# Kernel tuning notes

Measured on AMD Instinct MI355X. Metric: run time of the kernel, lower is better.

Reference implementation:

```python
import jax, jax.numpy as jnp
import numpy as np

NEG_INF = -1e9


def _rotate_half(x):
    h = x.shape[-1] // 2
    return jnp.concatenate([-x[..., h:], x[..., :h]], axis=-1)


def setup_inputs() -> dict:
    key = jax.random.key(0)
    ks = jax.random.split(key, 6)
    V, P, D, H = 4, 2048, 1280, 16
    hd = D // H
    return {
        "hidden_states": jax.random.normal(ks[0], (V, P, D), jnp.float32),
        "rope_cache": jax.random.normal(ks[1], (V, P, 1, 2 * hd), jnp.float32),
        "valid_lens": jax.random.randint(ks[2], (V,), 0, P, jnp.int32),
        "w_qkv": jax.random.normal(ks[3], (D, 3 * D), jnp.float32) * (D ** -0.5),
        "b_qkv": jnp.zeros((3 * D,), jnp.float32),
        "w_proj": jax.random.normal(ks[4], (D, D), jnp.float32) * (D ** -0.5),
        "b_proj": jnp.zeros((D,), jnp.float32),
        "n_heads": 16,
    }


def reference(hidden_states, rope_cache, valid_lens, w_qkv, b_qkv, w_proj, b_proj, n_heads):
    V, P, D = hidden_states.shape
    H = n_heads
    hd = D // H
    # fused QKV: (V, P, 3, H, hd)
    qkv = (hidden_states @ w_qkv + b_qkv).reshape(V, P, 3, H, hd)
    q, k, v = qkv[:, :, 0], qkv[:, :, 1], qkv[:, :, 2]  # each (V, P, H, hd)
    # 2D RoPE via precomputed cos/sin cache (V, P, 1, 2*hd)
    cos = rope_cache[..., :hd]
    sin = rope_cache[..., hd:]
    q = q * cos + _rotate_half(q) * sin
    k = k * cos + _rotate_half(k) * sin
    # attention with per-vision key padding mask (BlockMask equivalent)
    scale = hd ** -0.5
    scores = jnp.einsum("vqhd,vkhd->vhqk", q, k) * scale
    lens = jnp.maximum(valid_lens, 1)
    key_mask = jnp.arange(P)[None, :] < lens[:, None]  # (V, P)
    scores = jnp.where(key_mask[:, None, None, :], scores, NEG_INF)
    attn = jax.nn.softmax(scores, axis=-1)
    out = jnp.einsum("vhqk,vkhd->vqhd", attn, v).reshape(V, P, D)
    return out @ w_proj + b_proj
```

## Files before the change

### kernel.cpp

```cpp
#include <hip/hip_runtime.h>

typedef unsigned short u16;
typedef short bf16x8 __attribute__((ext_vector_type(8)));
typedef short s16x4 __attribute__((ext_vector_type(4)));
typedef float f32x4 __attribute__((ext_vector_type(4)));

#define DEV __device__ __forceinline__

DEV float b2f(u16 u) { union { unsigned i; float f; } x; x.i = ((unsigned)u) << 16; return x.f; }
DEV u16 f2b(float f) {
  union { float f; unsigned i; } x; x.f = f;
  unsigned r = x.i + 0x7fffu + ((x.i >> 16) & 1u);
  return (u16)(r >> 16);
}

DEV float exp2g(float x) { return __builtin_amdgcn_exp2f(x); }

#define GLDS(gp, lp) __builtin_amdgcn_global_load_lds( \
    (const __attribute__((address_space(1))) void*)(gp), \
    (__attribute__((address_space(3))) void*)(lp), 16, 0, 0)

constexpr float QSCALE = 0.11180339887498949f * 1.4426950408889634f;

__global__ __launch_bounds__(256) void prep_k(const float* __restrict__ hidden,
    u16* __restrict__ Ah, const float* __restrict__ wq, u16* __restrict__ Btq)
{
  __shared__ u16 tile[64 * 40];
  int b = blockIdx.x, tid = threadIdx.x;
  if (b < 5120) {
    int i = (b * 256 + tid) * 8;
    f32x4 a = *(const f32x4*)(hidden + i);
    f32x4 c = *(const f32x4*)(hidden + i + 4);
    bf16x8 o;
#pragma unroll
    for (int j = 0; j < 4; ++j) { o[j] = (short)f2b(a[j]); o[4 + j] = (short)f2b(c[j]); }
    *(bf16x8*)(Ah + i) = o;
  } else {
    int tb = b - 5120;
    int bx = tb % 60, by = tb / 60;
    const int Kd = 1280, Nd = 3840;
    int k0 = by * 32, n0 = bx * 64;
#pragma unroll
    for (int t = 0; t < 2; ++t) {
      int c = t * 256 + tid;
      int k_l = c >> 4, n_l = (c & 15) << 2;
      f32x4 vv = *(const f32x4*)(wq + (size_t)(k0 + k_l) * Nd + n0 + n_l);
#pragma unroll
      for (int j = 0; j < 4; ++j) tile[(n_l + j) * 40 + k_l] = f2b(vv[j]);
    }
    __syncthreads();
    int n_l = tid >> 2, kc = (tid & 3) << 3;
    bf16x8 vv = *(const bf16x8*)(tile + n_l * 40 + kc);
    *(bf16x8*)(Btq + (size_t)(n0 + n_l) * Kd + k0 + kc) = vv;
  }
}

template<int MODE>
__global__ __launch_bounds__(256) void gemm_k(const u16* __restrict__ A,
    const u16* __restrict__ Bt, const float* __restrict__ bias,
    u16* __restrict__ Oq, u16* __restrict__ Ok, u16* __restrict__ Ov,
    float* __restrict__ Of, int M, int N, int K)
{
  __shared__ u16 Asm[128 * 32];
  __shared__ u16 Bsm[128 * 32];
  const int tid = threadIdx.x;
  const int w = tid >> 6, lane = tid & 63, quad = lane >> 4, l16 = lane & 15;
  const int wm = w >> 1, wn = w & 1;
  const int m0 = blockIdx.y * 128, n0 = blockIdx.x * 128;
  const int srow0 = w * 32 + (lane >> 2);
  const int pchunk = lane & 3;

  const f32x4 zero4 = {0.f, 0.f, 0.f, 0.f};
  f32x4 acc[4][4];
#pragma unroll
  for (int i = 0; i < 4; ++i)
#pragma unroll
    for (int j = 0; j < 4; ++j) acc[i][j] = zero4;

  for (int k0 = 0; k0 < K; k0 += 32) {
    __syncthreads();
#pragma unroll
    for (int t = 0; t < 2; ++t) {
      int r = srow0 + t * 16;
      int q = pchunk ^ ((r >> 1) & 3);
      GLDS(A + (size_t)(m0 + r) * K + k0 + q * 8, Asm + r * 32 + pchunk * 8);
      GLDS(Bt + (size_t)(n0 + r) * K + k0 + q * 8, Bsm + r * 32 + pchunk * 8);
    }
    __syncthreads();
    bf16x8 af[4], bfr[4];
#pragma unroll
    for (int mi = 0; mi < 4; ++mi) {
      int lr = wm * 64 + mi * 16 + l16;
      af[mi] = *(const bf16x8*)(Asm + lr * 32 + ((quad ^ ((lr >> 1) & 3)) << 3));
    }
#pragma unroll
    for (int ni = 0; ni < 4; ++ni) {
      int nr = wn * 64 + ni * 16 + l16;
      bfr[ni] = *(const bf16x8*)(Bsm + nr * 32 + ((quad ^ ((nr >> 1) & 3)) << 3));
    }
#pragma unroll
    for (int mi = 0; mi < 4; ++mi)
#pragma unroll
      for (int ni = 0; ni < 4; ++ni)
        acc[mi][ni] = __builtin_amdgcn_mfma_f32_16x16x32_bf16(af[mi], bfr[ni], acc[mi][ni], 0, 0, 0);
  }

#pragma unroll
  for (int mi = 0; mi < 4; ++mi) {
#pragma unroll
    for (int ni = 0; ni < 4; ++ni) {
      int n = n0 + wn * 64 + ni * 16 + l16;
      float bb = bias[n];
#pragma unroll
      for (int r = 0; r < 4; ++r) {
        int m = m0 + wm * 64 + mi * 16 + quad * 4 + r;
        float val = acc[mi][ni][r] + bb;
        if (MODE == 0) {
          int t = n / 1280, rr = n - t * 1280;
          int hh = rr / 80, dd = rr - hh * 80;
          int vv = m >> 11, p = m & 2047;
          int vh = vv * 16 + hh;
          if (t == 0)      Oq[(size_t)(vh * 2048 + p) * 80 + dd] = f2b(val);
          else if (t == 1) Ok[(size_t)(vh * 2048 + p) * 80 + dd] = f2b(val);
          else             Ov[((size_t)vh * 80 + dd) * 2048 + p] = f2b(val);
        } else {
          Of[(size_t)m * N + n] = val;
        }
      }
    }
  }
}

__global__ __launch_bounds__(256) void rope_proj_k(u16* __restrict__ Q, u16* __restrict__ K,
    const float* __restrict__ rope, const float* __restrict__ wp, u16* __restrict__ Btp)
{
  __shared__ u16 tile[64 * 40];
  int b = blockIdx.x, tid = threadIdx.x;
  if (b < 40960) {
    constexpr int TOT = 4 * 16 * 2048 * 40;
    int idx = b * 256 + tid;
    int which = idx >= TOT ? 1 : 0;
    int r = which ? idx - TOT : idx;
    int d = r % 40;
    int t1 = r / 40;
    int p = t1 & 2047;
    int vv = t1 >> 15;
    u16* buf = which ? K : Q;
    size_t base = (size_t)t1 * 80;
    int rc = (vv * 2048 + p) * 160;
    float x0 = b2f(buf[base + d]), x1 = b2f(buf[base + d + 40]);
    float c0 = rope[rc + d], c1 = rope[rc + d + 40];
    float s0 = rope[rc + 80 + d], s1 = rope[rc + 80 + d + 40];
    float y0 = x0 * c0 - x1 * s0;
    float y1 = x1 * c1 + x0 * s1;
    if (!which) { y0 *= QSCALE; y1 *= QSCALE; }
    buf[base + d] = f2b(y0);
    buf[base + d + 40] = f2b(y1);
  } else {
    int tb = b - 40960;
    int bx = tb % 20, by = tb / 20;
    const int Kd = 1280, Nd = 1280;
    int k0 = by * 32, n0 = bx * 64;
#pragma unroll
    for (int t = 0; t < 2; ++t) {
      int c = t * 256 + tid;
      int k_l = c >> 4, n_l = (c & 15) << 2;
      f32x4 vv = *(const f32x4*)(wp + (size_t)(k0 + k_l) * Nd + n0 + n_l);
#pragma unroll
      for (int j = 0; j < 4; ++j) tile[(n_l + j) * 40 + k_l] = f2b(vv[j]);
    }
    __syncthreads();
    int n_l = tid >> 2, kc = (tid & 3) << 3;
    bf16x8 vv = *(const bf16x8*)(tile + n_l * 40 + kc);
    *(bf16x8*)(Btp + (size_t)(n0 + n_l) * Kd + k0 + kc) = vv;
  }
}

__global__ __launch_bounds__(256) void attn_k(const u16* __restrict__ Q,
    const u16* __restrict__ K, const u16* __restrict__ V,
    const int* __restrict__ lens, u16* __restrict__ O, const u16* __restrict__ zbuf)
{
  __shared__ u16 Ksm[64 * 96];
  __shared__ u16 Vt[96 * 64];
  __shared__ u16 Psm[4][16 * 72];
  const int v = blockIdx.z, h = blockIdx.y, q0 = blockIdx.x * 64;
  const int tid = threadIdx.x, w = tid >> 6, lane = tid & 63;
  const int quad = lane >> 4, l16 = lane & 15;
  int len = lens[v]; if (len < 1) len = 1;
  const int vh = v * 16 + h;

  if (tid < 128) {
    int row = 80 + (tid >> 3), pc = tid & 7;
    short val = (row == 80) ? (short)0x3F80 : (short)0;
    bf16x8 v8 = {val, val, val, val, val, val, val, val};
    *(bf16x8*)(Vt + row * 64 + pc * 8) = v8;
  }

  const bf16x8 zero8 = {0, 0, 0, 0, 0, 0, 0, 0};
  bf16x8 qf[3];
  {
    const u16* qp = Q + (size_t)(vh * 2048 + q0 + w * 16 + l16) * 80 + quad * 8;
    qf[0] = *(const bf16x8*)(qp);
    qf[1] = *(const bf16x8*)(qp + 32);
    qf[2] = (quad < 2) ? *(const bf16x8*)(qp + 64) : zero8;
  }

  const u16* kp[3]; int kstr[3];
#pragma unroll
  for (int t = 0; t < 3; ++t) {
    int L = w * 192 + t * 64 + lane;
    int key = L / 12, pc = L - key * 12;
    int q = (pc < 8) ? (pc ^ (key & 7)) : (8 + ((pc - 8) ^ (key & 3)));
    bool valid = q < 10;
    kp[t] = valid ? (K + (size_t)(vh * 2048 + key) * 80 + q * 8) : zbuf;
    kstr[t] = valid ? 5120 : 0;
  }
  const u16* vp[3];
#pragma unroll
  for (int t = 0; t < 3; ++t) {
    int seg = w + t * 4;
    int d = seg * 8 + (lane >> 3), pc = lane & 7;
    int q = pc ^ (d & 7);
    vp[t] = V + ((size_t)vh * 80 + d) * 2048 + q * 8;
  }

  const f32x4 zero4 = {0.f, 0.f, 0.f, 0.f};
  f32x4 o[6];
#pragma unroll
  for (int i = 0; i < 6; ++i) o[i] = zero4;
  float m_run[4] = {-3e38f, -3e38f, -3e38f, -3e38f};

  for (int key0 = 0; key0 < len; key0 += 64) {
    __syncthreads();
#pragma unroll
    for (int t = 0; t < 3; ++t) {
      GLDS(kp[t], Ksm + (w * 192 + t * 64) * 8);
      kp[t] += kstr[t];
    }
#pragma unroll
    for (int t = 0; t < 3; ++t) {
      int seg = w + t * 4;
      if (seg < 10) { GLDS(vp[t], Vt + seg * 512); vp[t] += 64; }
    }
    __syncthreads();

    f32x4 s[4];
#pragma unroll
    for (int i = 0; i < 4; ++i) s[i] = zero4;
#pragma unroll
    for (int ks = 0; ks < 3; ++ks) {
      int ph = (ks < 2) ? ((ks * 4 + quad) ^ (l16 & 7)) : (8 + (quad ^ (l16 & 3)));
#pragma unroll
      for (int ni = 0; ni < 4; ++ni) {
        bf16x8 kb = *(const bf16x8*)(Ksm + (ni * 16 + l16) * 96 + ph * 8);
        s[ni] = __builtin_amdgcn_mfma_f32_16x16x32_bf16(qf[ks], kb, s[ni], 0, 0, 0);
      }
    }
#pragma unroll
    for (int ni = 0; ni < 4; ++ni) {
      int key = key0 + ni * 16 + l16;
      if (key >= len) {
#pragma unroll
        for (int r = 0; r < 4; ++r) s[ni][r] = -1e9f;
      }
    }
    float mx[4];
#pragma unroll
    for (int r = 0; r < 4; ++r) mx[r] = fmaxf(fmaxf(s[0][r], s[1][r]), fmaxf(s[2][r], s[3][r]));
#pragma unroll
    for (int off = 1; off < 16; off <<= 1)
#pragma unroll
      for (int r = 0; r < 4; ++r) mx[r] = fmaxf(mx[r], __shfl_xor(mx[r], off, 64));
    float alpha[4];
#pragma unroll
    for (int r = 0; r < 4; ++r) {
      float mn = fmaxf(m_run[r], mx[r]);
      alpha[r] = exp2g(m_run[r] - mn);
      m_run[r] = mn;
    }
#pragma unroll
    for (int ni = 0; ni < 4; ++ni)
#pragma unroll
      for (int r = 0; r < 4; ++r) s[ni][r] = exp2g(s[ni][r] - m_run[r]);
#pragma unroll
    for (int ni = 0; ni < 4; ++ni)
#pragma unroll
      for (int r = 0; r < 4; ++r) {
        union { float f; unsigned u; } x; x.f = s[ni][r];
        Psm[w][(quad * 4 + r) * 72 + ni * 16 + l16] = (u16)(x.u >> 16);
      }
#pragma unroll
    for (int ni = 0; ni < 6; ++ni)
#pragma unroll
      for (int r = 0; r < 4; ++r) o[ni][r] *= alpha[r];
#pragma unroll
    for (int ks = 0; ks < 2; ++ks) {
      bf16x8 pa = *(const bf16x8*)(&Psm[w][l16 * 72 + ks * 32 + quad * 8]);
      int ph = (ks * 4 + quad) ^ (l16 & 7);
#pragma unroll
      for (int ni = 0; ni < 6; ++ni) {
        bf16x8 vb = *(const bf16x8*)(Vt + (ni * 16 + l16) * 64 + ph * 8);
        o[ni] = __builtin_amdgcn_mfma_f32_16x16x32_bf16(pa, vb, o[ni], 0, 0, 0);
      }
    }
  }
  float inv[4];
#pragma unroll
  for (int r = 0; r < 4; ++r) {
    float l = __shfl(o[5][r], (lane & 48), 64);
    inv[r] = 1.0f / l;
  }
#pragma unroll
  for (int ni = 0; ni < 5; ++ni)
#pragma unroll
    for (int r = 0; r < 4; ++r) {
      int qq = q0 + w * 16 + quad * 4 + r;
      O[((size_t)(v * 2048 + qq) * 16 + h) * 80 + ni * 16 + l16] = f2b(o[ni][r] * inv[r]);
    }
}

extern "C" void kernel_launch(void* const* d_in, const int* in_sizes, int n_in,
                              void* d_out, int out_size, void* d_ws, size_t ws_size,
                              hipStream_t stream) {
  const float* hidden = (const float*)d_in[0];
  const float* rope   = (const float*)d_in[1];
  const int*   lens   = (const int*)d_in[2];
  const float* w_qkv  = (const float*)d_in[3];
  const float* b_qkv  = (const float*)d_in[4];
  const float* w_proj = (const float*)d_in[5];
  const float* b_proj = (const float*)d_in[6];
  float* out = (float*)d_out;
  char* ws = (char*)d_ws;
  u16* Ah = (u16*)(ws);
  u16* Bt = (u16*)(ws + 20971520);
  u16* Qb = (u16*)(ws + 30801920);
  u16* Kb = (u16*)(ws + 51773440);
  u16* Vb = (u16*)(ws + 72744960);
  u16* At = Ah;
  u16* Bp = Bt;

  prep_k<<<7520, 256, 0, stream>>>(hidden, Ah, w_qkv, Bt);
  gemm_k<0><<<dim3(30, 64), 256, 0, stream>>>(Ah, Bt, b_qkv, Qb, Kb, Vb, nullptr, 8192, 3840, 1280);
  rope_proj_k<<<41760, 256, 0, stream>>>(Qb, Kb, rope, w_proj, Bp);
  attn_k<<<dim3(32, 16, 4), 256, 0, stream>>>(Qb, Kb, Vb, lens, At, (const u16*)b_qkv);
  gemm_k<1><<<dim3(10, 64), 256, 0, stream>>>(At, Bp, b_proj, nullptr, nullptr, nullptr, out, 8192, 1280, 1280);
}
```

Baseline: 455.0 us.

## Skip K/V projection tiles past valid length and deepen GEMM K-step to 64

The QKV GEMM now exits early for K and V output tiles whose row block lies entirely beyond the sequence's valid length, because those keys are masked out in attention anyway. Separately, the GEMM K-loop stages 64-wide K slices in LDS with a new 8-way XOR swizzle, halving the number of barrier pairs per tile. This costs twice the LDS per block, which may lower occupancy. The skip is correct only if the attention kernel never reads K/V rows past the clamped length.

```diff
diff --git a/kernel.cpp b/kernel.cpp
--- a/kernel.cpp
+++ b/kernel.cpp
@@ -2,7 +2,6 @@
 
 typedef unsigned short u16;
 typedef short bf16x8 __attribute__((ext_vector_type(8)));
-typedef short s16x4 __attribute__((ext_vector_type(4)));
 typedef float f32x4 __attribute__((ext_vector_type(4)));
 
 #define DEV __device__ __forceinline__
@@ -59,16 +58,24 @@
 __global__ __launch_bounds__(256) void gemm_k(const u16* __restrict__ A,
     const u16* __restrict__ Bt, const float* __restrict__ bias,
     u16* __restrict__ Oq, u16* __restrict__ Ok, u16* __restrict__ Ov,
-    float* __restrict__ Of, int M, int N, int K)
+    float* __restrict__ Of, const int* __restrict__ lens, int M, int N, int K)
 {
-  __shared__ u16 Asm[128 * 32];
-  __shared__ u16 Bsm[128 * 32];
+  __shared__ u16 Asm[128 * 64];
+  __shared__ u16 Bsm[128 * 64];
   const int tid = threadIdx.x;
   const int w = tid >> 6, lane = tid & 63, quad = lane >> 4, l16 = lane & 15;
   const int wm = w >> 1, wn = w & 1;
   const int m0 = blockIdx.y * 128, n0 = blockIdx.x * 128;
-  const int srow0 = w * 32 + (lane >> 2);
-  const int pchunk = lane & 3;
+
+  if (MODE == 0) {
+    if (n0 >= 1280) {
+      int vv = m0 >> 11, p0 = m0 & 2047;
+      int len = lens[vv]; if (len < 1) len = 1;
+      if (p0 >= len) return;
+    }
+  }
+
+  const int srow = tid >> 3, spc = tid & 7;
 
   const f32x4 zero4 = {0.f, 0.f, 0.f, 0.f};
   f32x4 acc[4][4];
@@ -77,32 +84,37 @@
 #pragma unroll
     for (int j = 0; j < 4; ++j) acc[i][j] = zero4;
 
-  for (int k0 = 0; k0 < K; k0 += 32) {
-    __syncthreads();
-#pragma unroll
-    for (int t = 0; t < 2; ++t) {
-      int r = srow0 + t * 16;
-      int q = pchunk ^ ((r >> 1) & 3);
-      GLDS(A + (size_t)(m0 + r) * K + k0 + q * 8, Asm + r * 32 + pchunk * 8);
-      GLDS(Bt + (size_t)(n0 + r) * K + k0 + q * 8, Bsm + r * 32 + pchunk * 8);
-    }
-    __syncthreads();
-    bf16x8 af[4], bfr[4];
-#pragma unroll
-    for (int mi = 0; mi < 4; ++mi) {
-      int lr = wm * 64 + mi * 16 + l16;
-      af[mi] = *(const bf16x8*)(Asm + lr * 32 + ((quad ^ ((lr >> 1) & 3)) << 3));
-    }
-#pragma unroll
-    for (int ni = 0; ni < 4; ++ni) {
-      int nr = wn * 64 + ni * 16 + l16;
-      bfr[ni] = *(const bf16x8*)(Bsm + nr * 32 + ((quad ^ ((nr >> 1) & 3)) << 3));
-    }
-#pragma unroll
-    for (int mi = 0; mi < 4; ++mi)
-#pragma unroll
-      for (int ni = 0; ni < 4; ++ni)
-        acc[mi][ni] = __builtin_amdgcn_mfma_f32_16x16x32_bf16(af[mi], bfr[ni], acc[mi][ni], 0, 0, 0);
+  for (int k0 = 0; k0 < K; k0 += 64) {
+    __syncthreads();
+#pragma unroll
+    for (int g = 0; g < 4; ++g) {
+      int r = g * 32 + srow;
+      int q = spc ^ (r & 7);
+      GLDS(A + (size_t)(m0 + r) * K + k0 + q * 8, Asm + r * 64 + spc * 8);
+      GLDS(Bt + (size_t)(n0 + r) * K + k0 + q * 8, Bsm + r * 64 + spc * 8);
+    }
+    __syncthreads();
+#pragma unroll
+    for (int ks = 0; ks < 2; ++ks) {
+      bf16x8 af[4], bfr[4];
+#pragma unroll
+      for (int mi = 0; mi < 4; ++mi) {
+        int lr = wm * 64 + mi * 16 + l16;
+        int ph = (ks * 4 + quad) ^ (lr & 7);
+        af[mi] = *(const bf16x8*)(Asm + lr * 64 + ph * 8);
+      }
+#pragma unroll
+      for (int ni = 0; ni < 4; ++ni) {
+        int nr = wn * 64 + ni * 16 + l16;
+        int ph = (ks * 4 + quad) ^ (nr & 7);
+        bfr[ni] = *(const bf16x8*)(Bsm + nr * 64 + ph * 8);
+      }
+#pragma unroll
+      for (int mi = 0; mi < 4; ++mi)
+#pragma unroll
+        for (int ni = 0; ni < 4; ++ni)
+          acc[mi][ni] = __builtin_amdgcn_mfma_f32_16x16x32_bf16(af[mi], bfr[ni], acc[mi][ni], 0, 0, 0);
+    }
   }
 
 #pragma unroll
@@ -340,8 +352,8 @@
   u16* Bp = Bt;
 
   prep_k<<<7520, 256, 0, stream>>>(hidden, Ah, w_qkv, Bt);
-  gemm_k<0><<<dim3(30, 64), 256, 0, stream>>>(Ah, Bt, b_qkv, Qb, Kb, Vb, nullptr, 8192, 3840, 1280);
+  gemm_k<0><<<dim3(30, 64), 256, 0, stream>>>(Ah, Bt, b_qkv, Qb, Kb, Vb, nullptr, lens, 8192, 3840, 1280);
   rope_proj_k<<<41760, 256, 0, stream>>>(Qb, Kb, rope, w_proj, Bp);
   attn_k<<<dim3(32, 16, 4), 256, 0, stream>>>(Qb, Kb, Vb, lens, At, (const u16*)b_qkv);
-  gemm_k<1><<<dim3(10, 64), 256, 0, stream>>>(At, Bp, b_proj, nullptr, nullptr, nullptr, out, 8192, 1280, 1280);
-}
+  gemm_k<1><<<dim3(10, 64), 256, 0, stream>>>(At, Bp, b_proj, nullptr, nullptr, nullptr, out, lens, 8192, 1280, 1280);
+}
```

New measurement: 402.7 us. 1.13x faster.
